# Kernel tuning notes

Hardware: AMD Instinct MI355X
Metric: run time of the kernel (lower is better)

Reference implementation:

```python
import jax, jax.numpy as jnp
import numpy as np
from jax import lax

B, N, T, NX = 4, 512, 24, 8
H = 64
PRED_LEN, NY = 12, 1
E_RAND = 8192
EPS = 1e-5


def setup_inputs() -> dict:
    key = jax.random.key(0)
    ks = jax.random.split(key, 24)
    sc = lambda k, shape: (jax.random.normal(k, shape, jnp.float32) * 0.05)
    x = jax.random.normal(ks[0], (B, N, T, NX), jnp.float32)
    er = jax.random.randint(ks[1], (2, E_RAND), 0, N, dtype=jnp.int32)
    loops = jnp.stack([jnp.arange(N, dtype=jnp.int32), jnp.arange(N, dtype=jnp.int32)])
    edge_index = jnp.concatenate([er, loops], axis=1)  # [2, 8704]
    return {
        'x': x,
        'edge_index': edge_index,
        'W_fc': sc(ks[2], (NX, H)), 'b_fc': jnp.zeros((H,), jnp.float32),
        'W1': sc(ks[3], (H, H)), 'a_l1': sc(ks[4], (H,)), 'a_r1': sc(ks[5], (H,)), 'bias1': jnp.zeros((H,), jnp.float32),
        'W2': sc(ks[6], (H, H)), 'a_l2': sc(ks[7], (H,)), 'a_r2': sc(ks[8], (H,)), 'bias2': jnp.zeros((H,), jnp.float32),
        'W_ih': sc(ks[9], (4 * H, H)), 'W_hh': sc(ks[10], (4 * H, H)),
        'b_ih': jnp.zeros((4 * H,), jnp.float32), 'b_hh': jnp.zeros((4 * H,), jnp.float32),
        'g_l': jnp.ones((H,), jnp.float32), 'b_l': jnp.zeros((H,), jnp.float32),
        'g_g': jnp.ones((H,), jnp.float32), 'b_g': jnp.zeros((H,), jnp.float32),
        'W_d': sc(ks[11], (H, PRED_LEN * NY)), 'b_d': jnp.zeros((PRED_LEN * NY,), jnp.float32),
    }


def _layer_norm(x, g, b):
    mu = jnp.mean(x, axis=-1, keepdims=True)
    var = jnp.mean(jnp.square(x - mu), axis=-1, keepdims=True)
    return (x - mu) * lax.rsqrt(var + EPS) * g + b


def _gat(x, W, a_l, a_r, bias, mask):
    # x: [B,N,T,F] -> operate in [B,T,N,H] layout (torch transpose(1,2))
    h = jnp.einsum('bntf,fh->btnh', x, W)          # [B,T,N,H]
    el = jnp.einsum('btnh,h->btn', h, a_l)          # attn_l
    er = jnp.einsum('btnh,h->btn', h, a_r)          # attn_r
    e = el[..., :, None] + er[..., None, :]         # [B,T,N,N]
    e = jax.nn.leaky_relu(e, negative_slope=0.2)
    e = jnp.where(mask, e, -jnp.inf)
    alpha = jax.nn.softmax(e, axis=-1)
    out = jnp.einsum('btmn,btnh->bmth', alpha, h) + bias  # back to [B,N,T,H]
    return jax.nn.gelu(out, approximate=False)


def _lstm(xseq, W_ih, W_hh, b_ih, b_hh):
    # xseq: [M, T, H] -> outputs [M, T, H]; PyTorch gate order i,f,g,o
    M = xseq.shape[0]
    Hh = W_hh.shape[1]
    b = b_ih + b_hh
    def step(carry, xt):
        hprev, cprev = carry
        gates = xt @ W_ih.T + hprev @ W_hh.T + b
        i, f, g, o = jnp.split(gates, 4, axis=-1)
        c = jax.nn.sigmoid(f) * cprev + jax.nn.sigmoid(i) * jnp.tanh(g)
        h = jax.nn.sigmoid(o) * jnp.tanh(c)
        return (h, c), h
    init = (jnp.zeros((M, Hh), xseq.dtype), jnp.zeros((M, Hh), xseq.dtype))
    _, hs = lax.scan(step, init, xseq.transpose(1, 0, 2))  # [T,M,H]
    return hs.transpose(1, 0, 2)


def reference(x, edge_index, W_fc, b_fc, W1, a_l1, a_r1, bias1, W2, a_l2, a_r2, bias2,
              W_ih, W_hh, b_ih, b_hh, g_l, b_l, g_g, b_g, W_d, b_d):
    Bb, Nn, Tt, _ = x.shape
    mask = jnp.zeros((Nn, Nn), bool).at[edge_index[0], edge_index[1]].set(True)
    x_h = jnp.einsum('bntf,fh->bnth', x, W_fc) + b_fc          # fc
    g1 = _gat(x_h, W1, a_l1, a_r1, bias1, mask)                # conv1
    g2 = _gat(g1, W2, a_l2, a_r2, bias2, mask)                 # conv2
    l = _lstm(x_h.reshape(Bb * Nn, Tt, -1), W_ih, W_hh, b_ih, b_hh).reshape(Bb, Nn, Tt, -1)
    h = _layer_norm(g2, g_g, b_g) + _layer_norm(l, g_l, b_l)
    last = h[:, :, -1, :]                                       # [B,N,H]
    out = last @ W_d + b_d                                      # [B,N,pred_len*ny]
    return out.reshape(Bb, Nn, PRED_LEN, NY)
```

## Files before the change

### kernel.cpp

```cpp
#include <hip/hip_runtime.h>
#include <hip/hip_bf16.h>
#include <math.h>

#define BB 4
#define NN 512
#define TT 24
#define NXF 8
#define HH 64
#define PRED 12
#define MM (BB*NN)

typedef __attribute__((ext_vector_type(8))) short short8;
typedef __attribute__((ext_vector_type(4))) float f32x4;
typedef unsigned short ushort;

#define WS_H1THI  0
#define WS_H1TLO  65536
#define WS_H2THI  131072
#define WS_H2TLO  196608
#define WS_HL     262144
#define WS_EL     393216
#define WS_ER     395264
#define WS_EL2    397312
#define WS_ER2    399360
#define WS_WCOMB  401408
#define WS_BCOMB  403456
#define WS_WHHFRAG 403712
#define WS_MASK   411904

__device__ inline float sigm(float x){ return 1.f/(1.f+__expf(-x)); }
__device__ inline float tanh_fast(float x){ float e=__expf(2.f*x); return 1.f - 2.f/(e+1.f); }
__device__ inline float gelu_exact(float x){ return 0.5f*x*(1.f+erff(x*0.70710678118654752440f)); }
__device__ inline ushort f2bu(float f){
    unsigned b=__float_as_uint(f);
    return (ushort)((b + 0x7FFFu + ((b>>16)&1u))>>16);
}
__device__ inline float bu2f(ushort u){ return __uint_as_float(((unsigned)u)<<16); }

__global__ __launch_bounds__(256,2) void gat1pre_kernel(
    const float* __restrict__ x, const float* __restrict__ Wfc, const float* __restrict__ bfc,
    const float* __restrict__ W1, const float* __restrict__ al1, const float* __restrict__ ar1,
    const float* __restrict__ Wih, const float* __restrict__ Whh,
    const float* __restrict__ bih, const float* __restrict__ bhh,
    const int* __restrict__ ei, int E,
    ushort* __restrict__ H1Thi, ushort* __restrict__ H1Tlo,
    float* __restrict__ el, float* __restrict__ er,
    float* __restrict__ wcombG, float* __restrict__ bcombG,
    ushort* __restrict__ whhfrag, unsigned* __restrict__ maskG)
{
    __shared__ float sw1[HH*HH];
    __shared__ float swfc[NXF*HH];
    __shared__ float sb[HH], sal[HH], sar[HH];
    __shared__ float sxh[4][68];
    __shared__ float sx[4][NXF];
    __shared__ unsigned msk[NN*16/2];
    const int t = threadIdx.x;

    if (blockIdx.x >= 520){
        for (int i = t; i < 8192; i += 256) msk[i] = 0u;
        __syncthreads();
        for (int e = t; e < E; e += 256){
            int s = ei[e];
            int d = ei[E + e];
            atomicOr(&msk[s*16 + (d>>5)], 1u << (d & 31));
        }
        __syncthreads();
        for (int i = t; i < 8192; i += 256) maskG[i] = msk[i];
        return;
    }

    if (blockIdx.x >= 512){
        const int f = blockIdx.x - 512;
        const int ng = t;
        float accf = 0.f, accb = 0.f;
        const float* wr = Wih + ng*64;
        #pragma unroll
        for (int k = 0; k < 64; ++k){
            float wv = wr[k];
            accf += Wfc[f*64 + k] * wv;
            accb += bfc[k] * wv;
        }
        wcombG[f*256 + ng] = accf;
        if (f == 0) bcombG[ng] = accb + bih[ng] + bhh[ng];
        #pragma unroll
        for (int u = 0; u < 8; ++u){
            int o = f*2048 + u*256 + t;
            int F  = o >> 9;
            int ln = (o >> 3) & 63;
            int j  = o & 7;
            int w_ = F >> 3, tt = (F >> 1) & 3, ks = F & 1;
            int q = ln >> 4, c = ln & 15;
            int ngx = (w_ + 4*tt)*16 + c;
            whhfrag[o] = f2bu(Whh[ngx*64 + ks*32 + q*8 + j]);
        }
        return;
    }

    const int r = t >> 6, h = t & 63;
    #pragma unroll
    for (int i = 0; i < 16; ++i) sw1[t + 256*i] = W1[t + 256*i];
    swfc[t] = Wfc[t];
    swfc[t+256] = Wfc[t+256];
    if (t < 64) sb[t] = bfc[t];
    else if (t < 128) sal[t-64] = al1[t-64];
    else if (t < 192) sar[t-128] = ar1[t-128];
    if (t < 32){
        int rr = t >> 3, f = t & 7;
        sx[rr][f] = x[(size_t)(blockIdx.x*4 + rr)*(TT*NXF) + (TT-1)*NXF + f];
    }
    __syncthreads();
    float xh = sb[h];
    #pragma unroll
    for (int f = 0; f < NXF; ++f) xh += sx[r][f]*swfc[f*HH + h];
    sxh[r][h] = xh;
    __syncthreads();
    float acc = 0.f;
    const float4* xr = (const float4*)&sxh[r][0];
    #pragma unroll
    for (int k4 = 0; k4 < 16; ++k4){
        float4 xv = xr[k4];
        acc += xv.x*sw1[(4*k4+0)*HH+h] + xv.y*sw1[(4*k4+1)*HH+h]
             + xv.z*sw1[(4*k4+2)*HH+h] + xv.w*sw1[(4*k4+3)*HH+h];
    }
    const int m = blockIdx.x*4 + r;
    {
        ushort hh = f2bu(acc);
        size_t o = ((size_t)(m >> 9)*HH + h)*NN + (m & (NN-1));
        H1Thi[o] = hh;
        H1Tlo[o] = f2bu(acc - bu2f(hh));
    }
    float v1 = acc*sal[h], v2 = acc*sar[h];
    #pragma unroll
    for (int o = 32; o; o >>= 1){ v1 += __shfl_xor(v1,o); v2 += __shfl_xor(v2,o); }
    if (h == 0){ el[m] = v1; er[m] = v2; }
}

#define LHS 72
#define LXS 40
__global__ __launch_bounds__(256,2) void mid_fused_kernel(
    const ushort* __restrict__ H1Thi, const ushort* __restrict__ H1Tlo,
    const float* __restrict__ el_in, const float* __restrict__ er_in,
    const unsigned* __restrict__ maskG,
    const float* __restrict__ bias1,
    const float* __restrict__ W2, const float* __restrict__ al2, const float* __restrict__ ar2,
    ushort* __restrict__ H2Thi, ushort* __restrict__ H2Tlo,
    float* __restrict__ el2, float* __restrict__ er2,
    const float* __restrict__ x,
    const float* __restrict__ wcombG, const float* __restrict__ bcombG,
    const ushort* __restrict__ whhfrag,
    float* __restrict__ hl)
{
    __shared__ __align__(16) char smem[41216];
    const int t = threadIdx.x;
    const int lane = t & 63;
    const int w = t >> 6;
    const int quad = lane >> 4;
    const int c16 = lane & 15;

    if (blockIdx.x >= 128){
        ushort* hbi = (ushort*)smem;
        ushort* hlo = (ushort*)(smem + 4608);
        ushort* xls = (ushort*)(smem + 9216);
        const int m0 = (blockIdx.x - 128) * 16;

        {
            unsigned* h0 = (unsigned*)hbi;
            unsigned* l0 = (unsigned*)hlo;
            for (int i = t; i < 2*16*LHS/2; i += 256){ h0[i] = 0u; l0[i] = 0u; }
            unsigned* xw = (unsigned*)xls;
            for (int i = t; i < TT*16*LXS/2; i += 256) xw[i] = 0u;
        }
        short8 bw[4][2]; short8 bx[4]; float bc[4];
        #pragma unroll
        for (int tt = 0; tt < 4; ++tt){
            const int ng = (w + 4*tt)*16 + c16;
            bc[tt] = bcombG[ng];
            #pragma unroll
            for (int ks = 0; ks < 2; ++ks)
                bw[tt][ks] = *(const short8*)&whhfrag[(((w*4+tt)*2)+ks)*512 + lane*8];
            short8 vx = {0,0,0,0,0,0,0,0};
            if (quad == 0){
                #pragma unroll
                for (int j = 0; j < 8; ++j) vx[j] = (short)f2bu(wcombG[j*256 + ng]);
            }
            bx[tt] = vx;
        }
        __syncthreads();
        for (int i = t; i < 16*TT*NXF; i += 256){
            int r = i / (TT*NXF);
            int rem = i - r*(TT*NXF);
            int st = rem >> 3, f = rem & 7;
            xls[st*(16*LXS) + r*LXS + f] = f2bu(x[(size_t)(m0+r)*(TT*NXF) + rem]);
        }
        __syncthreads();

        float cst[4] = {0,0,0,0};
        float hf[4]  = {0,0,0,0};

        for (int st = 0; st < TT; ++st){
            const int p = st & 1;
            const ushort* hb  = hbi + p*(16*LHS);
            const ushort* hl_ = hlo + p*(16*LHS);
            short8 ahi0 = *(const short8*)&hb[c16*LHS + quad*8];
            short8 ahi1 = *(const short8*)&hb[c16*LHS + 32 + quad*8];
            short8 alo0 = *(const short8*)&hl_[c16*LHS + quad*8];
            short8 alo1 = *(const short8*)&hl_[c16*LHS + 32 + quad*8];
            short8 ax   = *(const short8*)&xls[st*(16*LXS) + c16*LXS + quad*8];
            f32x4 acc[4];
            #pragma unroll
            for (int tt = 0; tt < 4; ++tt){
                f32x4 a = {bc[tt], bc[tt], bc[tt], bc[tt]};
                a = __builtin_amdgcn_mfma_f32_16x16x32_bf16(ax,   bx[tt],    a, 0,0,0);
                a = __builtin_amdgcn_mfma_f32_16x16x32_bf16(ahi0, bw[tt][0], a, 0,0,0);
                a = __builtin_amdgcn_mfma_f32_16x16x32_bf16(ahi1, bw[tt][1], a, 0,0,0);
                a = __builtin_amdgcn_mfma_f32_16x16x32_bf16(alo0, bw[tt][0], a, 0,0,0);
                a = __builtin_amdgcn_mfma_f32_16x16x32_bf16(alo1, bw[tt][1], a, 0,0,0);
                acc[tt] = a;
            }
            ushort* ho   = hbi + (p^1)*(16*LHS);
            ushort* lo_o = hlo + (p^1)*(16*LHS);
            #pragma unroll
            for (int reg = 0; reg < 4; ++reg){
                float gi = acc[0][reg], gf = acc[1][reg], gg = acc[2][reg], go = acc[3][reg];
                float cn = sigm(gf)*cst[reg] + sigm(gi)*tanh_fast(gg);
                cst[reg] = cn;
                float hn = sigm(go)*tanh_fast(cn);
                hf[reg] = hn;
                ushort hu = f2bu(hn);
                float lov = hn - bu2f(hu);
                int addr = (quad*4+reg)*LHS + w*16 + c16;
                ho[addr] = hu;
                lo_o[addr] = f2bu(lov);
            }
            __syncthreads();
        }
        #pragma unroll
        for (int reg = 0; reg < 4; ++reg)
            hl[(size_t)(m0 + quad*4 + reg)*HH + w*16 + c16] = hf[reg];
        return;
    }

    unsigned (*smask)[16] = (unsigned(*)[16])smem;
    float* er_s  = (float*)(smem + 1024);
    float* sal   = (float*)(smem + 3072);
    float* sar   = (float*)(smem + 3328);
    ushort (*ahi)[520] = (ushort(*)[520])(smem + 3584);
    ushort (*alo_)[520] = (ushort(*)[520])(smem + 20224);
    float (*xh2)[68] = (float(*)[68])(smem + 36864);
    float* sw2 = (float*)(smem + 3584);

    const int b = blockIdx.x >> 5;
    const int m0 = (blockIdx.x & 31) * 16;
    const int l = lane;

    if (t < 64) sal[t] = al2[t]; else if (t < 128) sar[t-64] = ar2[t-64];
    ((unsigned*)smask)[t] = maskG[m0*16 + t];
    er_s[t] = er_in[b*NN + t];
    er_s[t+256] = er_in[b*NN + t + 256];
    __syncthreads();
    for (int q = 0; q < 4; ++q){
        const int i = w*4 + q;
        const float elv = el_in[b*NN + m0 + i];
        float e8[8]; unsigned mk = 0; float mx = -1e30f;
        #pragma unroll
        for (int j = 0; j < 8; ++j){
            int n = l + 64*j;
            float ev = elv + er_s[n];
            ev = ev >= 0.f ? ev : 0.2f*ev;
            unsigned mb = (smask[i][(l>>5) + 2*j] >> (l & 31)) & 1u;
            e8[j] = ev;
            if (mb){ mk |= (1u<<j); mx = fmaxf(mx, ev); }
        }
        #pragma unroll
        for (int o = 32; o; o >>= 1) mx = fmaxf(mx, __shfl_xor(mx, o));
        float s = 0.f;
        #pragma unroll
        for (int j = 0; j < 8; ++j){
            float p = ((mk>>j) & 1u) ? __expf(e8[j]-mx) : 0.f;
            e8[j] = p; s += p;
        }
        #pragma unroll
        for (int o = 32; o; o >>= 1) s += __shfl_xor(s, o);
        const float inv = 1.f/s;
        #pragma unroll
        for (int j = 0; j < 8; ++j){
            float p = e8[j]*inv;
            ushort ph = f2bu(p);
            ahi[i][l + 64*j] = ph;
            alo_[i][l + 64*j] = f2bu(p - bu2f(ph));
        }
    }
    __syncthreads();

    f32x4 acc = {0.f,0.f,0.f,0.f};
    {
        const ushort* bhiP = H1Thi + ((size_t)b*HH + w*16 + c16)*NN + quad*8;
        const ushort* bloP = H1Tlo + ((size_t)b*HH + w*16 + c16)*NN + quad*8;
        const ushort* ahiP = &ahi[c16][quad*8];
        const ushort* aloP = &alo_[c16][quad*8];
        #pragma unroll
        for (int kk = 0; kk < 16; ++kk){
            short8 fa_hi = *(const short8*)(ahiP + kk*32);
            short8 fa_lo = *(const short8*)(aloP + kk*32);
            short8 fb_hi = *(const short8*)(bhiP + kk*32);
            short8 fb_lo = *(const short8*)(bloP + kk*32);
            acc = __builtin_amdgcn_mfma_f32_16x16x32_bf16(fa_hi, fb_hi, acc, 0,0,0);
            acc = __builtin_amdgcn_mfma_f32_16x16x32_bf16(fa_lo, fb_hi, acc, 0,0,0);
            acc = __builtin_amdgcn_mfma_f32_16x16x32_bf16(fa_hi, fb_lo, acc, 0,0,0);
        }
    }
    {
        const int h = w*16 + c16;
        const float bv = bias1[h];
        #pragma unroll
        for (int reg = 0; reg < 4; ++reg)
            xh2[quad*4 + reg][h] = gelu_exact(acc[reg] + bv);
    }
    __syncthreads();
    #pragma unroll
    for (int i = 0; i < 16; ++i) sw2[t + 256*i] = W2[t + 256*i];
    __syncthreads();
    {
        const int h = l;
        for (int q = 0; q < 4; ++q){
            const int i = w + 4*q;
            float acc2 = 0.f;
            const float4* xr = (const float4*)&xh2[i][0];
            #pragma unroll
            for (int k4 = 0; k4 < 16; ++k4){
                float4 xv = xr[k4];
                acc2 += xv.x*sw2[(4*k4+0)*HH+h] + xv.y*sw2[(4*k4+1)*HH+h]
                      + xv.z*sw2[(4*k4+2)*HH+h] + xv.w*sw2[(4*k4+3)*HH+h];
            }
            const int m = m0 + i;
            {
                ushort vh = f2bu(acc2);
                size_t o = ((size_t)b*HH + h)*NN + m;
                H2Thi[o] = vh;
                H2Tlo[o] = f2bu(acc2 - bu2f(vh));
            }
            float v1 = acc2*sal[h], v2 = acc2*sar[h];
            #pragma unroll
            for (int o = 32; o; o >>= 1){ v1 += __shfl_xor(v1,o); v2 += __shfl_xor(v2,o); }
            if (h == 0){ el2[b*NN + m] = v1; er2[b*NN + m] = v2; }
        }
    }
}

__global__ __launch_bounds__(256,2) void attn2_final_kernel(
    const ushort* __restrict__ H2Thi, const ushort* __restrict__ H2Tlo,
    const float* __restrict__ el_in, const float* __restrict__ er_in,
    const unsigned* __restrict__ maskG,
    const float* __restrict__ bias2,
    const float* __restrict__ hl,
    const float* __restrict__ g_l, const float* __restrict__ b_l,
    const float* __restrict__ g_g, const float* __restrict__ b_g,
    const float* __restrict__ W_d, const float* __restrict__ b_d,
    float* __restrict__ out)
{
    __shared__ __align__(16) char smem[40448];
    unsigned (*smask)[16] = (unsigned(*)[16])smem;
    float* er_s  = (float*)(smem + 1024);
    ushort (*ahi)[520] = (ushort(*)[520])(smem + 3072);
    ushort (*alo_)[520] = (ushort(*)[520])(smem + 19712);
    float* sg2  = (float*)(smem + 36352);
    float* sdec = (float*)(smem + 3072);

    const int t = threadIdx.x;
    const int b = blockIdx.x >> 5;
    const int m0 = (blockIdx.x & 31) * 16;
    const int l = t & 63, w = t >> 6;
    const int quad = l >> 4, c16 = l & 15;

    ((unsigned*)smask)[t] = maskG[m0*16 + t];
    er_s[t] = er_in[b*NN + t];
    er_s[t+256] = er_in[b*NN + t + 256];
    __syncthreads();
    for (int q = 0; q < 4; ++q){
        const int i = w*4 + q;
        const float elv = el_in[b*NN + m0 + i];
        float e8[8]; unsigned mk = 0; float mx = -1e30f;
        #pragma unroll
        for (int j = 0; j < 8; ++j){
            int n = l + 64*j;
            float ev = elv + er_s[n];
            ev = ev >= 0.f ? ev : 0.2f*ev;
            unsigned mb = (smask[i][(l>>5) + 2*j] >> (l & 31)) & 1u;
            e8[j] = ev;
            if (mb){ mk |= (1u<<j); mx = fmaxf(mx, ev); }
        }
        #pragma unroll
        for (int o = 32; o; o >>= 1) mx = fmaxf(mx, __shfl_xor(mx, o));
        float s = 0.f;
        #pragma unroll
        for (int j = 0; j < 8; ++j){
            float p = ((mk>>j) & 1u) ? __expf(e8[j]-mx) : 0.f;
            e8[j] = p; s += p;
        }
        #pragma unroll
        for (int o = 32; o; o >>= 1) s += __shfl_xor(s, o);
        const float inv = 1.f/s;
        #pragma unroll
        for (int j = 0; j < 8; ++j){
            float p = e8[j]*inv;
            ushort ph = f2bu(p);
            ahi[i][l + 64*j] = ph;
            alo_[i][l + 64*j] = f2bu(p - bu2f(ph));
        }
    }
    __syncthreads();

    f32x4 acc = {0.f,0.f,0.f,0.f};
    {
        const ushort* bhiP = H2Thi + ((size_t)b*HH + w*16 + c16)*NN + quad*8;
        const ushort* bloP = H2Tlo + ((size_t)b*HH + w*16 + c16)*NN + quad*8;
        const ushort* ahiP = &ahi[c16][quad*8];
        const ushort* aloP = &alo_[c16][quad*8];
        #pragma unroll
        for (int kk = 0; kk < 16; ++kk){
            short8 fa_hi = *(const short8*)(ahiP + kk*32);
            short8 fa_lo = *(const short8*)(aloP + kk*32);
            short8 fb_hi = *(const short8*)(bhiP + kk*32);
            short8 fb_lo = *(const short8*)(bloP + kk*32);
            acc = __builtin_amdgcn_mfma_f32_16x16x32_bf16(fa_hi, fb_hi, acc, 0,0,0);
            acc = __builtin_amdgcn_mfma_f32_16x16x32_bf16(fa_lo, fb_hi, acc, 0,0,0);
            acc = __builtin_amdgcn_mfma_f32_16x16x32_bf16(fa_hi, fb_lo, acc, 0,0,0);
        }
    }
    {
        const int h = w*16 + c16;
        const float bv = bias2[h];
        #pragma unroll
        for (int reg = 0; reg < 4; ++reg)
            sg2[(quad*4 + reg)*HH + h] = gelu_exact(acc[reg] + bv);
    }
    __syncthreads();
    const int gbase = b*NN + m0;
    {
        const int h = l;
        for (int q = 0; q < 4; ++q){
            const int ml = w*4 + q;
            float gv = sg2[ml*HH + h];
            float lv = hl[(size_t)(gbase + ml)*HH + h];

            float s1 = gv;
            #pragma unroll
            for (int o = 32; o; o >>= 1) s1 += __shfl_xor(s1, o);
            float dg = gv - s1*(1.f/64.f);
            float v1 = dg*dg;
            #pragma unroll
            for (int o = 32; o; o >>= 1) v1 += __shfl_xor(v1, o);
            float lng = dg*rsqrtf(v1*(1.f/64.f) + 1e-5f)*g_g[h] + b_g[h];

            float s2 = lv;
            #pragma unroll
            for (int o = 32; o; o >>= 1) s2 += __shfl_xor(s2, o);
            float dl = lv - s2*(1.f/64.f);
            float v2 = dl*dl;
            #pragma unroll
            for (int o = 32; o; o >>= 1) v2 += __shfl_xor(v2, o);
            float lnl = dl*rsqrtf(v2*(1.f/64.f) + 1e-5f)*g_l[h] + b_l[h];

            sdec[ml*HH + h] = lng + lnl;
        }
    }
    __syncthreads();
    if (t < 16*PRED){
        int rr = t / PRED, pp = t - rr*PRED;
        float a = b_d[pp];
        #pragma unroll
        for (int k = 0; k < HH; ++k) a += sdec[rr*HH + k]*W_d[k*PRED + pp];
        out[(size_t)(gbase + rr)*PRED + pp] = a;
    }
}

extern "C" void kernel_launch(void* const* d_in, const int* in_sizes, int n_in,
                              void* d_out, int out_size, void* d_ws, size_t ws_size,
                              hipStream_t stream){
    const float* x    = (const float*)d_in[0];
    const int*   ei   = (const int*)  d_in[1];
    const float* Wfc  = (const float*)d_in[2];
    const float* bfc  = (const float*)d_in[3];
    const float* W1   = (const float*)d_in[4];
    const float* al1  = (const float*)d_in[5];
    const float* ar1  = (const float*)d_in[6];
    const float* bias1= (const float*)d_in[7];
    const float* W2   = (const float*)d_in[8];
    const float* al2  = (const float*)d_in[9];
    const float* ar2  = (const float*)d_in[10];
    const float* bias2= (const float*)d_in[11];
    const float* Wih  = (const float*)d_in[12];
    const float* Whh  = (const float*)d_in[13];
    const float* bih  = (const float*)d_in[14];
    const float* bhh  = (const float*)d_in[15];
    const float* g_l  = (const float*)d_in[16];
    const float* b_l  = (const float*)d_in[17];
    const float* g_g  = (const float*)d_in[18];
    const float* b_g  = (const float*)d_in[19];
    const float* W_d  = (const float*)d_in[20];
    const float* b_d  = (const float*)d_in[21];

    float* ws = (float*)d_ws;
    const int E = in_sizes[1] / 2;

    gat1pre_kernel<<<521, 256, 0, stream>>>(x, Wfc, bfc, W1, al1, ar1,
                                            Wih, Whh, bih, bhh,
                                            ei, E,
                                            (ushort*)(ws+WS_H1THI), (ushort*)(ws+WS_H1TLO),
                                            ws+WS_EL, ws+WS_ER,
                                            ws+WS_WCOMB, ws+WS_BCOMB,
                                            (ushort*)(ws+WS_WHHFRAG),
                                            (unsigned*)(ws+WS_MASK));
    mid_fused_kernel<<<256, 256, 0, stream>>>((const ushort*)(ws+WS_H1THI), (const ushort*)(ws+WS_H1TLO),
                                              ws+WS_EL, ws+WS_ER,
                                              (const unsigned*)(ws+WS_MASK),
                                              bias1, W2, al2, ar2,
                                              (ushort*)(ws+WS_H2THI), (ushort*)(ws+WS_H2TLO),
                                              ws+WS_EL2, ws+WS_ER2,
                                              x, ws+WS_WCOMB, ws+WS_BCOMB,
                                              (const ushort*)(ws+WS_WHHFRAG),
                                              ws+WS_HL);
    attn2_final_kernel<<<BB*(NN/16), 256, 0, stream>>>((const ushort*)(ws+WS_H2THI), (const ushort*)(ws+WS_H2TLO),
                                                       ws+WS_EL2, ws+WS_ER2,
                                                       (const unsigned*)(ws+WS_MASK),
                                                       bias2, ws+WS_HL,
                                                       g_l, b_l, g_g, b_g, W_d, b_d,
                                                       (float*)d_out);
}
```

Before: 152.7 us.

## Fuse three kernels into one persistent kernel with atomic grid barriers

Replaces the three-kernel pipeline with one 257-block kernel plus a tiny counter-reset kernel. Blocks sync through global atomic counters: a grid barrier separates the two GAT stages, and the attention blocks wait for the LSTM blocks only before the final layer norm. Each LSTM block now builds its own bf16 Whh fragments and the combined input weights instead of reading precomputed workspace copies, so that work runs in parallel with GAT. This removes launch gaps and lets the LSTM overlap both attention stages, but all 257 blocks must be co-resident or the spin-waits deadlock, and the per-block weight prep is repeated work.

```diff
diff --git a/kernel.cpp b/kernel.cpp
--- a/kernel.cpp
+++ b/kernel.cpp
@@ -8,7 +8,6 @@
 #define NXF 8
 #define HH 64
 #define PRED 12
-#define MM (BB*NN)
 
 typedef __attribute__((ext_vector_type(8))) short short8;
 typedef __attribute__((ext_vector_type(4))) float f32x4;
@@ -23,10 +22,8 @@
 #define WS_ER     395264
 #define WS_EL2    397312
 #define WS_ER2    399360
-#define WS_WCOMB  401408
-#define WS_BCOMB  403456
-#define WS_WHHFRAG 403712
-#define WS_MASK   411904
+#define WS_MASK   401408
+#define WS_CTR    409600
 
 __device__ inline float sigm(float x){ return 1.f/(1.f+__expf(-x)); }
 __device__ inline float tanh_fast(float x){ float e=__expf(2.f*x); return 1.f - 2.f/(e+1.f); }
@@ -37,153 +34,129 @@
 }
 __device__ inline float bu2f(ushort u){ return __uint_as_float(((unsigned)u)<<16); }
 
-__global__ __launch_bounds__(256,2) void gat1pre_kernel(
-    const float* __restrict__ x, const float* __restrict__ Wfc, const float* __restrict__ bfc,
+__device__ inline void fence_arrive(unsigned* c){ __threadfence(); atomicAdd(c, 1u); }
+__device__ inline void wait_count(unsigned* c, unsigned tgt){
+    while (__hip_atomic_load(c, __ATOMIC_RELAXED, __HIP_MEMORY_SCOPE_AGENT) < tgt)
+        __builtin_amdgcn_s_sleep(2);
+    __threadfence();
+}
+__device__ inline void grid_bar(unsigned* c, unsigned tgt){
+    __syncthreads();
+    if (threadIdx.x == 0){ fence_arrive(c); wait_count(c, tgt); }
+    __syncthreads();
+}
+
+__global__ void init_ctr_kernel(unsigned* c){ c[threadIdx.x] = 0u; }
+
+#define LHS 72
+#define LXS 40
+__global__ __launch_bounds__(256,2) void fused_kernel(
+    const float* __restrict__ x, const int* __restrict__ ei, int E,
+    const float* __restrict__ Wfc, const float* __restrict__ bfc,
     const float* __restrict__ W1, const float* __restrict__ al1, const float* __restrict__ ar1,
+    const float* __restrict__ bias1,
+    const float* __restrict__ W2, const float* __restrict__ al2, const float* __restrict__ ar2,
+    const float* __restrict__ bias2,
     const float* __restrict__ Wih, const float* __restrict__ Whh,
     const float* __restrict__ bih, const float* __restrict__ bhh,
-    const int* __restrict__ ei, int E,
+    const float* __restrict__ g_l, const float* __restrict__ b_l,
+    const float* __restrict__ g_g, const float* __restrict__ b_g,
+    const float* __restrict__ W_d, const float* __restrict__ b_d,
     ushort* __restrict__ H1Thi, ushort* __restrict__ H1Tlo,
-    float* __restrict__ el, float* __restrict__ er,
-    float* __restrict__ wcombG, float* __restrict__ bcombG,
-    ushort* __restrict__ whhfrag, unsigned* __restrict__ maskG)
+    ushort* __restrict__ H2Thi, ushort* __restrict__ H2Tlo,
+    float* __restrict__ hl,
+    float* __restrict__ elG, float* __restrict__ erG,
+    float* __restrict__ el2G, float* __restrict__ er2G,
+    unsigned* __restrict__ maskG, unsigned* __restrict__ ctr,
+    float* __restrict__ out)
 {
-    __shared__ float sw1[HH*HH];
-    __shared__ float swfc[NXF*HH];
-    __shared__ float sb[HH], sal[HH], sar[HH];
-    __shared__ float sxh[4][68];
-    __shared__ float sx[4][NXF];
-    __shared__ unsigned msk[NN*16/2];
-    const int t = threadIdx.x;
-
-    if (blockIdx.x >= 520){
-        for (int i = t; i < 8192; i += 256) msk[i] = 0u;
-        __syncthreads();
-        for (int e = t; e < E; e += 256){
-            int s = ei[e];
-            int d = ei[E + e];
-            atomicOr(&msk[s*16 + (d>>5)], 1u << (d & 31));
-        }
-        __syncthreads();
-        for (int i = t; i < 8192; i += 256) maskG[i] = msk[i];
-        return;
-    }
-
-    if (blockIdx.x >= 512){
-        const int f = blockIdx.x - 512;
-        const int ng = t;
-        float accf = 0.f, accb = 0.f;
-        const float* wr = Wih + ng*64;
-        #pragma unroll
-        for (int k = 0; k < 64; ++k){
-            float wv = wr[k];
-            accf += Wfc[f*64 + k] * wv;
-            accb += bfc[k] * wv;
-        }
-        wcombG[f*256 + ng] = accf;
-        if (f == 0) bcombG[ng] = accb + bih[ng] + bhh[ng];
-        #pragma unroll
-        for (int u = 0; u < 8; ++u){
-            int o = f*2048 + u*256 + t;
-            int F  = o >> 9;
-            int ln = (o >> 3) & 63;
-            int j  = o & 7;
-            int w_ = F >> 3, tt = (F >> 1) & 3, ks = F & 1;
-            int q = ln >> 4, c = ln & 15;
-            int ngx = (w_ + 4*tt)*16 + c;
-            whhfrag[o] = f2bu(Whh[ngx*64 + ks*32 + q*8 + j]);
-        }
-        return;
-    }
-
-    const int r = t >> 6, h = t & 63;
-    #pragma unroll
-    for (int i = 0; i < 16; ++i) sw1[t + 256*i] = W1[t + 256*i];
-    swfc[t] = Wfc[t];
-    swfc[t+256] = Wfc[t+256];
-    if (t < 64) sb[t] = bfc[t];
-    else if (t < 128) sal[t-64] = al1[t-64];
-    else if (t < 192) sar[t-128] = ar1[t-128];
-    if (t < 32){
-        int rr = t >> 3, f = t & 7;
-        sx[rr][f] = x[(size_t)(blockIdx.x*4 + rr)*(TT*NXF) + (TT-1)*NXF + f];
-    }
-    __syncthreads();
-    float xh = sb[h];
-    #pragma unroll
-    for (int f = 0; f < NXF; ++f) xh += sx[r][f]*swfc[f*HH + h];
-    sxh[r][h] = xh;
-    __syncthreads();
-    float acc = 0.f;
-    const float4* xr = (const float4*)&sxh[r][0];
-    #pragma unroll
-    for (int k4 = 0; k4 < 16; ++k4){
-        float4 xv = xr[k4];
-        acc += xv.x*sw1[(4*k4+0)*HH+h] + xv.y*sw1[(4*k4+1)*HH+h]
-             + xv.z*sw1[(4*k4+2)*HH+h] + xv.w*sw1[(4*k4+3)*HH+h];
-    }
-    const int m = blockIdx.x*4 + r;
-    {
-        ushort hh = f2bu(acc);
-        size_t o = ((size_t)(m >> 9)*HH + h)*NN + (m & (NN-1));
-        H1Thi[o] = hh;
-        H1Tlo[o] = f2bu(acc - bu2f(hh));
-    }
-    float v1 = acc*sal[h], v2 = acc*sar[h];
-    #pragma unroll
-    for (int o = 32; o; o >>= 1){ v1 += __shfl_xor(v1,o); v2 += __shfl_xor(v2,o); }
-    if (h == 0){ el[m] = v1; er[m] = v2; }
-}
-
-#define LHS 72
-#define LXS 40
-__global__ __launch_bounds__(256,2) void mid_fused_kernel(
-    const ushort* __restrict__ H1Thi, const ushort* __restrict__ H1Tlo,
-    const float* __restrict__ el_in, const float* __restrict__ er_in,
-    const unsigned* __restrict__ maskG,
-    const float* __restrict__ bias1,
-    const float* __restrict__ W2, const float* __restrict__ al2, const float* __restrict__ ar2,
-    ushort* __restrict__ H2Thi, ushort* __restrict__ H2Tlo,
-    float* __restrict__ el2, float* __restrict__ er2,
-    const float* __restrict__ x,
-    const float* __restrict__ wcombG, const float* __restrict__ bcombG,
-    const ushort* __restrict__ whhfrag,
-    float* __restrict__ hl)
-{
-    __shared__ __align__(16) char smem[41216];
+    __shared__ __align__(16) char smem[49152];
     const int t = threadIdx.x;
     const int lane = t & 63;
     const int w = t >> 6;
     const int quad = lane >> 4;
     const int c16 = lane & 15;
-
-    if (blockIdx.x >= 128){
+    const int blk = blockIdx.x;
+
+    if (blk == 256){
+        unsigned* msk = (unsigned*)smem;
+        for (int i = t; i < 8192; i += 256) msk[i] = 0u;
+        __syncthreads();
+        for (int e = t; e < E; e += 256){
+            int s = ei[e];
+            int d = ei[E + e];
+            atomicOr(&msk[s*16 + (d>>5)], 1u << (d & 31));
+        }
+        __syncthreads();
+        for (int i = t; i < 8192; i += 256) maskG[i] = msk[i];
+        __syncthreads();
+        if (t == 0) fence_arrive(ctr + 0);
+        return;
+    }
+
+    if (blk >= 128){
+        const int m0 = (blk - 128) * 16;
+        float* sWfcL = (float*)smem;
+        float* sbfc  = (float*)(smem + 2048);
+        sWfcL[t] = Wfc[t]; sWfcL[t+256] = Wfc[t+256];
+        if (t < 64) sbfc[t] = bfc[t];
+        __syncthreads();
+
+        short8 bw[4][2]; short8 bx[4]; float bc[4];
+        #pragma unroll
+        for (int tt = 0; tt < 4; ++tt){
+            const int ng = (w + 4*tt)*16 + c16;
+            #pragma unroll
+            for (int ks = 0; ks < 2; ++ks){
+                const float* wp = Whh + (size_t)ng*64 + ks*32 + quad*8;
+                short8 v;
+                #pragma unroll
+                for (int j = 0; j < 8; ++j) v[j] = (short)f2bu(wp[j]);
+                bw[tt][ks] = v;
+            }
+        }
+        {
+            const int myng = (w + 4*quad)*16 + c16;
+            float accj[8] = {0,0,0,0,0,0,0,0};
+            float accb = 0.f;
+            const float4* wr4 = (const float4*)(Wih + (size_t)myng*64);
+            #pragma unroll
+            for (int k4 = 0; k4 < 16; ++k4){
+                float4 wv = wr4[k4];
+                accb += sbfc[4*k4+0]*wv.x; accb += sbfc[4*k4+1]*wv.y;
+                accb += sbfc[4*k4+2]*wv.z; accb += sbfc[4*k4+3]*wv.w;
+                #pragma unroll
+                for (int j = 0; j < 8; ++j){
+                    accj[j] += sWfcL[j*64+4*k4+0]*wv.x;
+                    accj[j] += sWfcL[j*64+4*k4+1]*wv.y;
+                    accj[j] += sWfcL[j*64+4*k4+2]*wv.z;
+                    accj[j] += sWfcL[j*64+4*k4+3]*wv.w;
+                }
+            }
+            accb += bih[myng] + bhh[myng];
+            #pragma unroll
+            for (int tt = 0; tt < 4; ++tt){
+                bc[tt] = __shfl(accb, tt*16 + c16);
+                short8 vx = {0,0,0,0,0,0,0,0};
+                #pragma unroll
+                for (int j = 0; j < 8; ++j){
+                    float wv = __shfl(accj[j], tt*16 + c16);
+                    if (quad == 0) vx[j] = (short)f2bu(wv);
+                }
+                bx[tt] = vx;
+            }
+        }
+        __syncthreads();
+
         ushort* hbi = (ushort*)smem;
         ushort* hlo = (ushort*)(smem + 4608);
         ushort* xls = (ushort*)(smem + 9216);
-        const int m0 = (blockIdx.x - 128) * 16;
-
         {
             unsigned* h0 = (unsigned*)hbi;
             unsigned* l0 = (unsigned*)hlo;
             for (int i = t; i < 2*16*LHS/2; i += 256){ h0[i] = 0u; l0[i] = 0u; }
             unsigned* xw = (unsigned*)xls;
             for (int i = t; i < TT*16*LXS/2; i += 256) xw[i] = 0u;
-        }
-        short8 bw[4][2]; short8 bx[4]; float bc[4];
-        #pragma unroll
-        for (int tt = 0; tt < 4; ++tt){
-            const int ng = (w + 4*tt)*16 + c16;
-            bc[tt] = bcombG[ng];
-            #pragma unroll
-            for (int ks = 0; ks < 2; ++ks)
-                bw[tt][ks] = *(const short8*)&whhfrag[(((w*4+tt)*2)+ks)*512 + lane*8];
-            short8 vx = {0,0,0,0,0,0,0,0};
-            if (quad == 0){
-                #pragma unroll
-                for (int j = 0; j < 8; ++j) vx[j] = (short)f2bu(wcombG[j*256 + ng]);
-            }
-            bx[tt] = vx;
         }
         __syncthreads();
         for (int i = t; i < 16*TT*NXF; i += 256){
@@ -237,240 +210,300 @@
         #pragma unroll
         for (int reg = 0; reg < 4; ++reg)
             hl[(size_t)(m0 + quad*4 + reg)*HH + w*16 + c16] = hf[reg];
+        __syncthreads();
+        if (t == 0) fence_arrive(ctr + 32);
         return;
     }
 
-    unsigned (*smask)[16] = (unsigned(*)[16])smem;
-    float* er_s  = (float*)(smem + 1024);
-    float* sal   = (float*)(smem + 3072);
-    float* sar   = (float*)(smem + 3328);
-    ushort (*ahi)[520] = (ushort(*)[520])(smem + 3584);
-    ushort (*alo_)[520] = (ushort(*)[520])(smem + 20224);
-    float (*xh2)[68] = (float(*)[68])(smem + 36864);
-    float* sw2 = (float*)(smem + 3584);
-
-    const int b = blockIdx.x >> 5;
-    const int m0 = (blockIdx.x & 31) * 16;
-    const int l = lane;
-
-    if (t < 64) sal[t] = al2[t]; else if (t < 128) sar[t-64] = ar2[t-64];
-    ((unsigned*)smask)[t] = maskG[m0*16 + t];
-    er_s[t] = er_in[b*NN + t];
-    er_s[t+256] = er_in[b*NN + t + 256];
-    __syncthreads();
-    for (int q = 0; q < 4; ++q){
-        const int i = w*4 + q;
-        const float elv = el_in[b*NN + m0 + i];
-        float e8[8]; unsigned mk = 0; float mx = -1e30f;
-        #pragma unroll
-        for (int j = 0; j < 8; ++j){
-            int n = l + 64*j;
-            float ev = elv + er_s[n];
-            ev = ev >= 0.f ? ev : 0.2f*ev;
-            unsigned mb = (smask[i][(l>>5) + 2*j] >> (l & 31)) & 1u;
-            e8[j] = ev;
-            if (mb){ mk |= (1u<<j); mx = fmaxf(mx, ev); }
-        }
-        #pragma unroll
-        for (int o = 32; o; o >>= 1) mx = fmaxf(mx, __shfl_xor(mx, o));
-        float s = 0.f;
-        #pragma unroll
-        for (int j = 0; j < 8; ++j){
-            float p = ((mk>>j) & 1u) ? __expf(e8[j]-mx) : 0.f;
-            e8[j] = p; s += p;
-        }
-        #pragma unroll
-        for (int o = 32; o; o >>= 1) s += __shfl_xor(s, o);
-        const float inv = 1.f/s;
-        #pragma unroll
-        for (int j = 0; j < 8; ++j){
-            float p = e8[j]*inv;
-            ushort ph = f2bu(p);
-            ahi[i][l + 64*j] = ph;
-            alo_[i][l + 64*j] = f2bu(p - bu2f(ph));
-        }
-    }
-    __syncthreads();
-
-    f32x4 acc = {0.f,0.f,0.f,0.f};
+    const int b   = blk >> 5;
+    const int m0l = (blk & 31) * 16;
+    const int m0g = blk * 16;
+
     {
-        const ushort* bhiP = H1Thi + ((size_t)b*HH + w*16 + c16)*NN + quad*8;
-        const ushort* bloP = H1Tlo + ((size_t)b*HH + w*16 + c16)*NN + quad*8;
-        const ushort* ahiP = &ahi[c16][quad*8];
-        const ushort* aloP = &alo_[c16][quad*8];
-        #pragma unroll
-        for (int kk = 0; kk < 16; ++kk){
-            short8 fa_hi = *(const short8*)(ahiP + kk*32);
-            short8 fa_lo = *(const short8*)(aloP + kk*32);
-            short8 fb_hi = *(const short8*)(bhiP + kk*32);
-            short8 fb_lo = *(const short8*)(bloP + kk*32);
-            acc = __builtin_amdgcn_mfma_f32_16x16x32_bf16(fa_hi, fb_hi, acc, 0,0,0);
-            acc = __builtin_amdgcn_mfma_f32_16x16x32_bf16(fa_lo, fb_hi, acc, 0,0,0);
-            acc = __builtin_amdgcn_mfma_f32_16x16x32_bf16(fa_hi, fb_lo, acc, 0,0,0);
-        }
-    }
-    {
-        const int h = w*16 + c16;
-        const float bv = bias1[h];
-        #pragma unroll
-        for (int reg = 0; reg < 4; ++reg)
-            xh2[quad*4 + reg][h] = gelu_exact(acc[reg] + bv);
-    }
-    __syncthreads();
-    #pragma unroll
-    for (int i = 0; i < 16; ++i) sw2[t + 256*i] = W2[t + 256*i];
-    __syncthreads();
-    {
-        const int h = l;
-        for (int q = 0; q < 4; ++q){
-            const int i = w + 4*q;
-            float acc2 = 0.f;
-            const float4* xr = (const float4*)&xh2[i][0];
+        float* sw1  = (float*)smem;
+        float* swfc = (float*)(smem + 16384);
+        float* sb   = (float*)(smem + 18432);
+        float* sal  = (float*)(smem + 18688);
+        float* sar  = (float*)(smem + 18944);
+        float (*sx)[NXF] = (float(*)[NXF])(smem + 19200);
+        float (*sxh)[68] = (float(*)[68])(smem + 19712);
+        ushort (*thi)[68] = (ushort(*)[68])(smem + 24064);
+        ushort (*tlo)[68] = (ushort(*)[68])(smem + 26240);
+
+        #pragma unroll
+        for (int i = 0; i < 16; ++i) sw1[t + 256*i] = W1[t + 256*i];
+        swfc[t] = Wfc[t];
+        swfc[t+256] = Wfc[t+256];
+        if (t < 64) sb[t] = bfc[t];
+        else if (t < 128) sal[t-64] = al1[t-64];
+        else if (t < 192) sar[t-128] = ar1[t-128];
+        if (t < 128){
+            int rr = t >> 3, f = t & 7;
+            sx[rr][f] = x[(size_t)(m0g + rr)*(TT*NXF) + (TT-1)*NXF + f];
+        }
+        __syncthreads();
+        #pragma unroll
+        for (int rr = 0; rr < 4; ++rr){
+            const int row = w*4 + rr;
+            float v = sb[lane];
+            #pragma unroll
+            for (int f = 0; f < NXF; ++f) v += sx[row][f]*swfc[f*HH + lane];
+            sxh[row][lane] = v;
+        }
+        __syncthreads();
+        #pragma unroll
+        for (int rr = 0; rr < 4; ++rr){
+            const int row = w*4 + rr;
+            float acc = 0.f;
+            const float4* xr = (const float4*)&sxh[row][0];
             #pragma unroll
             for (int k4 = 0; k4 < 16; ++k4){
                 float4 xv = xr[k4];
-                acc2 += xv.x*sw2[(4*k4+0)*HH+h] + xv.y*sw2[(4*k4+1)*HH+h]
-                      + xv.z*sw2[(4*k4+2)*HH+h] + xv.w*sw2[(4*k4+3)*HH+h];
-            }
-            const int m = m0 + i;
-            {
+                acc += xv.x*sw1[(4*k4+0)*HH+lane] + xv.y*sw1[(4*k4+1)*HH+lane]
+                     + xv.z*sw1[(4*k4+2)*HH+lane] + xv.w*sw1[(4*k4+3)*HH+lane];
+            }
+            ushort hh = f2bu(acc);
+            thi[row][lane] = hh;
+            tlo[row][lane] = f2bu(acc - bu2f(hh));
+            float v1 = acc*sal[lane], v2 = acc*sar[lane];
+            #pragma unroll
+            for (int o = 32; o; o >>= 1){ v1 += __shfl_xor(v1,o); v2 += __shfl_xor(v2,o); }
+            if (lane == 0){ elG[m0g + row] = v1; erG[m0g + row] = v2; }
+        }
+        __syncthreads();
+        #pragma unroll
+        for (int p = 0; p < 4; ++p){
+            int hh2 = (t >> 4) + 16*p, n2 = t & 15;
+            size_t og = ((size_t)b*HH + hh2)*NN + m0l + n2;
+            H1Thi[og] = thi[n2][hh2];
+            H1Tlo[og] = tlo[n2][hh2];
+        }
+    }
+    grid_bar(ctr + 0, 129);
+
+    {
+        unsigned (*smask)[16] = (unsigned(*)[16])smem;
+        float* er_s  = (float*)(smem + 1024);
+        float* sal   = (float*)(smem + 3072);
+        float* sar   = (float*)(smem + 3328);
+        ushort (*ahi)[520] = (ushort(*)[520])(smem + 3584);
+        ushort (*alo_)[520] = (ushort(*)[520])(smem + 20224);
+        float (*xh2)[68] = (float(*)[68])(smem + 36864);
+        ushort (*th2)[68] = (ushort(*)[68])(smem + 41216);
+        ushort (*tl2)[68] = (ushort(*)[68])(smem + 43392);
+        float* sw2 = (float*)(smem + 3584);
+        const int l = lane;
+
+        if (t < 64) sal[t] = al2[t]; else if (t < 128) sar[t-64] = ar2[t-64];
+        ((unsigned*)smask)[t] = maskG[m0l*16 + t];
+        er_s[t] = erG[b*NN + t];
+        er_s[t+256] = erG[b*NN + t + 256];
+        __syncthreads();
+        for (int q = 0; q < 4; ++q){
+            const int i = w*4 + q;
+            const float elv = elG[b*NN + m0l + i];
+            float e8[8]; unsigned mk = 0; float mx = -1e30f;
+            #pragma unroll
+            for (int j = 0; j < 8; ++j){
+                int n = l + 64*j;
+                float ev = elv + er_s[n];
+                ev = ev >= 0.f ? ev : 0.2f*ev;
+                unsigned mb = (smask[i][(l>>5) + 2*j] >> (l & 31)) & 1u;
+                e8[j] = ev;
+                if (mb){ mk |= (1u<<j); mx = fmaxf(mx, ev); }
+            }
+            #pragma unroll
+            for (int o = 32; o; o >>= 1) mx = fmaxf(mx, __shfl_xor(mx, o));
+            float s = 0.f;
+            #pragma unroll
+            for (int j = 0; j < 8; ++j){
+                float p = ((mk>>j) & 1u) ? __expf(e8[j]-mx) : 0.f;
+                e8[j] = p; s += p;
+            }
+            #pragma unroll
+            for (int o = 32; o; o >>= 1) s += __shfl_xor(s, o);
+            const float inv = 1.f/s;
+            #pragma unroll
+            for (int j = 0; j < 8; ++j){
+                float p = e8[j]*inv;
+                ushort ph = f2bu(p);
+                ahi[i][l + 64*j] = ph;
+                alo_[i][l + 64*j] = f2bu(p - bu2f(ph));
+            }
+        }
+        __syncthreads();
+
+        f32x4 acc = {0.f,0.f,0.f,0.f};
+        {
+            const ushort* bhiP = H1Thi + ((size_t)b*HH + w*16 + c16)*NN + quad*8;
+            const ushort* bloP = H1Tlo + ((size_t)b*HH + w*16 + c16)*NN + quad*8;
+            const ushort* ahiP = &ahi[c16][quad*8];
+            const ushort* aloP = &alo_[c16][quad*8];
+            #pragma unroll
+            for (int kk = 0; kk < 16; ++kk){
+                short8 fa_hi = *(const short8*)(ahiP + kk*32);
+                short8 fa_lo = *(const short8*)(aloP + kk*32);
+                short8 fb_hi = *(const short8*)(bhiP + kk*32);
+                short8 fb_lo = *(const short8*)(bloP + kk*32);
+                acc = __builtin_amdgcn_mfma_f32_16x16x32_bf16(fa_hi, fb_hi, acc, 0,0,0);
+                acc = __builtin_amdgcn_mfma_f32_16x16x32_bf16(fa_lo, fb_hi, acc, 0,0,0);
+                acc = __builtin_amdgcn_mfma_f32_16x16x32_bf16(fa_hi, fb_lo, acc, 0,0,0);
+            }
+        }
+        {
+            const int h = w*16 + c16;
+            const float bv = bias1[h];
+            #pragma unroll
+            for (int reg = 0; reg < 4; ++reg)
+                xh2[quad*4 + reg][h] = gelu_exact(acc[reg] + bv);
+        }
+        __syncthreads();
+        #pragma unroll
+        for (int i = 0; i < 16; ++i) sw2[t + 256*i] = W2[t + 256*i];
+        __syncthreads();
+        {
+            const int h = l;
+            for (int q = 0; q < 4; ++q){
+                const int i = w + 4*q;
+                float acc2 = 0.f;
+                const float4* xr = (const float4*)&xh2[i][0];
+                #pragma unroll
+                for (int k4 = 0; k4 < 16; ++k4){
+                    float4 xv = xr[k4];
+                    acc2 += xv.x*sw2[(4*k4+0)*HH+h] + xv.y*sw2[(4*k4+1)*HH+h]
+                          + xv.z*sw2[(4*k4+2)*HH+h] + xv.w*sw2[(4*k4+3)*HH+h];
+                }
                 ushort vh = f2bu(acc2);
-                size_t o = ((size_t)b*HH + h)*NN + m;
-                H2Thi[o] = vh;
-                H2Tlo[o] = f2bu(acc2 - bu2f(vh));
-            }
-            float v1 = acc2*sal[h], v2 = acc2*sar[h];
-            #pragma unroll
-            for (int o = 32; o; o >>= 1){ v1 += __shfl_xor(v1,o); v2 += __shfl_xor(v2,o); }
-            if (h == 0){ el2[b*NN + m] = v1; er2[b*NN + m] = v2; }
+                th2[i][h] = vh;
+                tl2[i][h] = f2bu(acc2 - bu2f(vh));
+                float v1 = acc2*sal[h], v2 = acc2*sar[h];
+                #pragma unroll
+                for (int o = 32; o; o >>= 1){ v1 += __shfl_xor(v1,o); v2 += __shfl_xor(v2,o); }
+                if (h == 0){ el2G[b*NN + m0l + i] = v1; er2G[b*NN + m0l + i] = v2; }
+            }
+        }
+        __syncthreads();
+        #pragma unroll
+        for (int p = 0; p < 4; ++p){
+            int hh2 = (t >> 4) + 16*p, n2 = t & 15;
+            size_t og = ((size_t)b*HH + hh2)*NN + m0l + n2;
+            H2Thi[og] = th2[n2][hh2];
+            H2Tlo[og] = tl2[n2][hh2];
         }
     }
-}
-
-__global__ __launch_bounds__(256,2) void attn2_final_kernel(
-    const ushort* __restrict__ H2Thi, const ushort* __restrict__ H2Tlo,
-    const float* __restrict__ el_in, const float* __restrict__ er_in,
-    const unsigned* __restrict__ maskG,
-    const float* __restrict__ bias2,
-    const float* __restrict__ hl,
-    const float* __restrict__ g_l, const float* __restrict__ b_l,
-    const float* __restrict__ g_g, const float* __restrict__ b_g,
-    const float* __restrict__ W_d, const float* __restrict__ b_d,
-    float* __restrict__ out)
-{
-    __shared__ __align__(16) char smem[40448];
-    unsigned (*smask)[16] = (unsigned(*)[16])smem;
-    float* er_s  = (float*)(smem + 1024);
-    ushort (*ahi)[520] = (ushort(*)[520])(smem + 3072);
-    ushort (*alo_)[520] = (ushort(*)[520])(smem + 19712);
-    float* sg2  = (float*)(smem + 36352);
-    float* sdec = (float*)(smem + 3072);
-
-    const int t = threadIdx.x;
-    const int b = blockIdx.x >> 5;
-    const int m0 = (blockIdx.x & 31) * 16;
-    const int l = t & 63, w = t >> 6;
-    const int quad = l >> 4, c16 = l & 15;
-
-    ((unsigned*)smask)[t] = maskG[m0*16 + t];
-    er_s[t] = er_in[b*NN + t];
-    er_s[t+256] = er_in[b*NN + t + 256];
-    __syncthreads();
-    for (int q = 0; q < 4; ++q){
-        const int i = w*4 + q;
-        const float elv = el_in[b*NN + m0 + i];
-        float e8[8]; unsigned mk = 0; float mx = -1e30f;
-        #pragma unroll
-        for (int j = 0; j < 8; ++j){
-            int n = l + 64*j;
-            float ev = elv + er_s[n];
-            ev = ev >= 0.f ? ev : 0.2f*ev;
-            unsigned mb = (smask[i][(l>>5) + 2*j] >> (l & 31)) & 1u;
-            e8[j] = ev;
-            if (mb){ mk |= (1u<<j); mx = fmaxf(mx, ev); }
-        }
-        #pragma unroll
-        for (int o = 32; o; o >>= 1) mx = fmaxf(mx, __shfl_xor(mx, o));
-        float s = 0.f;
-        #pragma unroll
-        for (int j = 0; j < 8; ++j){
-            float p = ((mk>>j) & 1u) ? __expf(e8[j]-mx) : 0.f;
-            e8[j] = p; s += p;
-        }
-        #pragma unroll
-        for (int o = 32; o; o >>= 1) s += __shfl_xor(s, o);
-        const float inv = 1.f/s;
-        #pragma unroll
-        for (int j = 0; j < 8; ++j){
-            float p = e8[j]*inv;
-            ushort ph = f2bu(p);
-            ahi[i][l + 64*j] = ph;
-            alo_[i][l + 64*j] = f2bu(p - bu2f(ph));
-        }
-    }
-    __syncthreads();
-
-    f32x4 acc = {0.f,0.f,0.f,0.f};
+    grid_bar(ctr + 16, 128);
+
     {
-        const ushort* bhiP = H2Thi + ((size_t)b*HH + w*16 + c16)*NN + quad*8;
-        const ushort* bloP = H2Tlo + ((size_t)b*HH + w*16 + c16)*NN + quad*8;
-        const ushort* ahiP = &ahi[c16][quad*8];
-        const ushort* aloP = &alo_[c16][quad*8];
-        #pragma unroll
-        for (int kk = 0; kk < 16; ++kk){
-            short8 fa_hi = *(const short8*)(ahiP + kk*32);
-            short8 fa_lo = *(const short8*)(aloP + kk*32);
-            short8 fb_hi = *(const short8*)(bhiP + kk*32);
-            short8 fb_lo = *(const short8*)(bloP + kk*32);
-            acc = __builtin_amdgcn_mfma_f32_16x16x32_bf16(fa_hi, fb_hi, acc, 0,0,0);
-            acc = __builtin_amdgcn_mfma_f32_16x16x32_bf16(fa_lo, fb_hi, acc, 0,0,0);
-            acc = __builtin_amdgcn_mfma_f32_16x16x32_bf16(fa_hi, fb_lo, acc, 0,0,0);
-        }
-    }
-    {
-        const int h = w*16 + c16;
-        const float bv = bias2[h];
-        #pragma unroll
-        for (int reg = 0; reg < 4; ++reg)
-            sg2[(quad*4 + reg)*HH + h] = gelu_exact(acc[reg] + bv);
-    }
-    __syncthreads();
-    const int gbase = b*NN + m0;
-    {
-        const int h = l;
+        unsigned (*smask)[16] = (unsigned(*)[16])smem;
+        float* er_s  = (float*)(smem + 1024);
+        ushort (*ahi)[520] = (ushort(*)[520])(smem + 3072);
+        ushort (*alo_)[520] = (ushort(*)[520])(smem + 19712);
+        float* sg2  = (float*)(smem + 36352);
+        float* sdec = (float*)(smem + 3072);
+        const int l = lane;
+
+        ((unsigned*)smask)[t] = maskG[m0l*16 + t];
+        er_s[t] = er2G[b*NN + t];
+        er_s[t+256] = er2G[b*NN + t + 256];
+        __syncthreads();
         for (int q = 0; q < 4; ++q){
-            const int ml = w*4 + q;
-            float gv = sg2[ml*HH + h];
-            float lv = hl[(size_t)(gbase + ml)*HH + h];
-
-            float s1 = gv;
-            #pragma unroll
-            for (int o = 32; o; o >>= 1) s1 += __shfl_xor(s1, o);
-            float dg = gv - s1*(1.f/64.f);
-            float v1 = dg*dg;
-            #pragma unroll
-            for (int o = 32; o; o >>= 1) v1 += __shfl_xor(v1, o);
-            float lng = dg*rsqrtf(v1*(1.f/64.f) + 1e-5f)*g_g[h] + b_g[h];
-
-            float s2 = lv;
-            #pragma unroll
-            for (int o = 32; o; o >>= 1) s2 += __shfl_xor(s2, o);
-            float dl = lv - s2*(1.f/64.f);
-            float v2 = dl*dl;
-            #pragma unroll
-            for (int o = 32; o; o >>= 1) v2 += __shfl_xor(v2, o);
-            float lnl = dl*rsqrtf(v2*(1.f/64.f) + 1e-5f)*g_l[h] + b_l[h];
-
-            sdec[ml*HH + h] = lng + lnl;
-        }
-    }
-    __syncthreads();
-    if (t < 16*PRED){
-        int rr = t / PRED, pp = t - rr*PRED;
-        float a = b_d[pp];
-        #pragma unroll
-        for (int k = 0; k < HH; ++k) a += sdec[rr*HH + k]*W_d[k*PRED + pp];
-        out[(size_t)(gbase + rr)*PRED + pp] = a;
+            const int i = w*4 + q;
+            const float elv = el2G[b*NN + m0l + i];
+            float e8[8]; unsigned mk = 0; float mx = -1e30f;
+            #pragma unroll
+            for (int j = 0; j < 8; ++j){
+                int n = l + 64*j;
+                float ev = elv + er_s[n];
+                ev = ev >= 0.f ? ev : 0.2f*ev;
+                unsigned mb = (smask[i][(l>>5) + 2*j] >> (l & 31)) & 1u;
+                e8[j] = ev;
+                if (mb){ mk |= (1u<<j); mx = fmaxf(mx, ev); }
+            }
+            #pragma unroll
+            for (int o = 32; o; o >>= 1) mx = fmaxf(mx, __shfl_xor(mx, o));
+            float s = 0.f;
+            #pragma unroll
+            for (int j = 0; j < 8; ++j){
+                float p = ((mk>>j) & 1u) ? __expf(e8[j]-mx) : 0.f;
+                e8[j] = p; s += p;
+            }
+            #pragma unroll
+            for (int o = 32; o; o >>= 1) s += __shfl_xor(s, o);
+            const float inv = 1.f/s;
+            #pragma unroll
+            for (int j = 0; j < 8; ++j){
+                float p = e8[j]*inv;
+                ushort ph = f2bu(p);
+                ahi[i][l + 64*j] = ph;
+                alo_[i][l + 64*j] = f2bu(p - bu2f(ph));
+            }
+        }
+        __syncthreads();
+
+        f32x4 acc = {0.f,0.f,0.f,0.f};
+        {
+            const ushort* bhiP = H2Thi + ((size_t)b*HH + w*16 + c16)*NN + quad*8;
+            const ushort* bloP = H2Tlo + ((size_t)b*HH + w*16 + c16)*NN + quad*8;
+            const ushort* ahiP = &ahi[c16][quad*8];
+            const ushort* aloP = &alo_[c16][quad*8];
+            #pragma unroll
+            for (int kk = 0; kk < 16; ++kk){
+                short8 fa_hi = *(const short8*)(ahiP + kk*32);
+                short8 fa_lo = *(const short8*)(aloP + kk*32);
+                short8 fb_hi = *(const short8*)(bhiP + kk*32);
+                short8 fb_lo = *(const short8*)(bloP + kk*32);
+                acc = __builtin_amdgcn_mfma_f32_16x16x32_bf16(fa_hi, fb_hi, acc, 0,0,0);
+                acc = __builtin_amdgcn_mfma_f32_16x16x32_bf16(fa_lo, fb_hi, acc, 0,0,0);
+                acc = __builtin_amdgcn_mfma_f32_16x16x32_bf16(fa_hi, fb_lo, acc, 0,0,0);
+            }
+        }
+        {
+            const int h = w*16 + c16;
+            const float bv = bias2[h];
+            #pragma unroll
+            for (int reg = 0; reg < 4; ++reg)
+                sg2[(quad*4 + reg)*HH + h] = gelu_exact(acc[reg] + bv);
+        }
+        __syncthreads();
+        if (t == 0) wait_count(ctr + 32, 128);
+        __syncthreads();
+        const int gbase = b*NN + m0l;
+        {
+            const int h = l;
+            for (int q = 0; q < 4; ++q){
+                const int ml = w*4 + q;
+                float gv = sg2[ml*HH + h];
+                float lv = hl[(size_t)(gbase + ml)*HH + h];
+
+                float s1 = gv;
+                #pragma unroll
+                for (int o = 32; o; o >>= 1) s1 += __shfl_xor(s1, o);
+                float dg = gv - s1*(1.f/64.f);
+                float v1 = dg*dg;
+                #pragma unroll
+                for (int o = 32; o; o >>= 1) v1 += __shfl_xor(v1, o);
+                float lng = dg*rsqrtf(v1*(1.f/64.f) + 1e-5f)*g_g[h] + b_g[h];
+
+                float s2 = lv;
+                #pragma unroll
+                for (int o = 32; o; o >>= 1) s2 += __shfl_xor(s2, o);
+                float dl = lv - s2*(1.f/64.f);
+                float v2 = dl*dl;
+                #pragma unroll
+                for (int o = 32; o; o >>= 1) v2 += __shfl_xor(v2, o);
+                float lnl = dl*rsqrtf(v2*(1.f/64.f) + 1e-5f)*g_l[h] + b_l[h];
+
+                sdec[ml*HH + h] = lng + lnl;
+            }
+        }
+        __syncthreads();
+        if (t < 16*PRED){
+            int rr = t / PRED, pp = t - rr*PRED;
+            float a = b_d[pp];
+            #pragma unroll
+            for (int k = 0; k < HH; ++k) a += sdec[rr*HH + k]*W_d[k*PRED + pp];
+            out[(size_t)(gbase + rr)*PRED + pp] = a;
+        }
     }
 }
 
@@ -502,28 +535,16 @@
 
     float* ws = (float*)d_ws;
     const int E = in_sizes[1] / 2;
-
-    gat1pre_kernel<<<521, 256, 0, stream>>>(x, Wfc, bfc, W1, al1, ar1,
-                                            Wih, Whh, bih, bhh,
-                                            ei, E,
-                                            (ushort*)(ws+WS_H1THI), (ushort*)(ws+WS_H1TLO),
-                                            ws+WS_EL, ws+WS_ER,
-                                            ws+WS_WCOMB, ws+WS_BCOMB,
-                                            (ushort*)(ws+WS_WHHFRAG),
-                                            (unsigned*)(ws+WS_MASK));
-    mid_fused_kernel<<<256, 256, 0, stream>>>((const ushort*)(ws+WS_H1THI), (const ushort*)(ws+WS_H1TLO),
-                                              ws+WS_EL, ws+WS_ER,
-                                              (const unsigned*)(ws+WS_MASK),
-                                              bias1, W2, al2, ar2,
-                                              (ushort*)(ws+WS_H2THI), (ushort*)(ws+WS_H2TLO),
-                                              ws+WS_EL2, ws+WS_ER2,
-                                              x, ws+WS_WCOMB, ws+WS_BCOMB,
-                                              (const ushort*)(ws+WS_WHHFRAG),
-                                              ws+WS_HL);
-    attn2_final_kernel<<<BB*(NN/16), 256, 0, stream>>>((const ushort*)(ws+WS_H2THI), (const ushort*)(ws+WS_H2TLO),
-                                                       ws+WS_EL2, ws+WS_ER2,
-                                                       (const unsigned*)(ws+WS_MASK),
-                                                       bias2, ws+WS_HL,
-                                                       g_l, b_l, g_g, b_g, W_d, b_d,
-                                                       (float*)d_out);
+    unsigned* ctr = (unsigned*)(ws + WS_CTR);
+
+    init_ctr_kernel<<<1, 64, 0, stream>>>(ctr);
+    fused_kernel<<<257, 256, 0, stream>>>(
+        x, ei, E, Wfc, bfc, W1, al1, ar1, bias1, W2, al2, ar2, bias2,
+        Wih, Whh, bih, bhh, g_l, b_l, g_g, b_g, W_d, b_d,
+        (ushort*)(ws+WS_H1THI), (ushort*)(ws+WS_H1TLO),
+        (ushort*)(ws+WS_H2THI), (ushort*)(ws+WS_H2TLO),
+        ws+WS_HL,
+        ws+WS_EL, ws+WS_ER, ws+WS_EL2, ws+WS_ER2,
+        (unsigned*)(ws+WS_MASK), ctr,
+        (float*)d_out);
 }
```

New measurement: 157.9 us. 1.03x slower.
